# Kernel tuning notes

Measured on AMD Instinct MI355X. Metric: run time of the kernel, lower is better.

Reference implementation:

```python
import jax, jax.numpy as jnp
import numpy as np
from jax import lax

NUM_TAGS = 9
HIDDEN = 768
BATCH = 64
SEQ = 512


def setup_inputs() -> dict:
    key = jax.random.key(0)
    ks = jax.random.split(key, 6)
    hidden = jax.random.normal(ks[0], (BATCH, SEQ, HIDDEN), dtype=jnp.float32)
    labels = jax.random.randint(ks[1], (BATCH, SEQ), 0, NUM_TAGS)  # all >= 0 -> full mask
    weight = jax.random.normal(ks[2], (NUM_TAGS, HIDDEN), dtype=jnp.float32) * 0.02
    bias = jnp.zeros((NUM_TAGS,), dtype=jnp.float32)
    start_transitions = jax.random.normal(ks[3], (NUM_TAGS,), dtype=jnp.float32) * 0.1
    end_transitions = jax.random.normal(ks[4], (NUM_TAGS,), dtype=jnp.float32) * 0.1
    transitions = jax.random.normal(ks[5], (NUM_TAGS, NUM_TAGS), dtype=jnp.float32) * 0.1
    return dict(hidden=hidden, labels=labels, weight=weight, bias=bias,
                start_transitions=start_transitions, end_transitions=end_transitions,
                transitions=transitions)


def _crf_log_likelihood(emissions, tags, mask, start_t, end_t, trans):
    """pytorch-crf log-likelihood, reduction='sum'.
    emissions [B,L,T] float, tags [B,L] int, mask [B,L] bool."""
    # --- numerator: score of the gold path ---
    tag0 = tags[:, 0]
    score0 = start_t[tag0] + jnp.take_along_axis(emissions[:, 0], tag0[:, None], axis=1)[:, 0]

    def num_step(carry, inp):
        score, prev = carry
        em, tg, m = inp  # em [B,T], tg [B], m [B]
        s = trans[prev, tg] + jnp.take_along_axis(em, tg[:, None], axis=1)[:, 0]
        score = score + jnp.where(m, s, jnp.zeros_like(s))
        prev = jnp.where(m, tg, prev)
        return (score, prev), None

    (num_score, last_tag), _ = lax.scan(
        num_step, (score0, tag0),
        (emissions[:, 1:].swapaxes(0, 1), tags[:, 1:].T, mask[:, 1:].T))
    numerator = num_score + end_t[last_tag]

    # --- denominator: forward algorithm (log-sum-exp recurrence) ---
    alpha0 = start_t[None, :] + emissions[:, 0]  # [B,T]

    def den_step(alpha, inp):
        em, m = inp  # em [B,T], m [B]
        nxt = jax.nn.logsumexp(alpha[:, :, None] + trans[None], axis=1) + em
        alpha = jnp.where(m[:, None], nxt, alpha)
        return alpha, None

    alpha, _ = lax.scan(den_step, alpha0,
                        (emissions[:, 1:].swapaxes(0, 1), mask[:, 1:].T))
    denominator = jax.nn.logsumexp(alpha + end_t[None, :], axis=1)

    return jnp.sum(numerator - denominator)


def _viterbi_decode(emissions, mask, start_t, end_t, trans):
    """Max-plus DP + backtrack. Returns padded [B,L] int32 best tag sequence."""
    B, L, T = emissions.shape
    score0 = start_t[None, :] + emissions[:, 0]  # [B,T]
    identity = jnp.arange(T, dtype=jnp.int32)[None, :]  # identity backpointer for masked steps

    def fwd_step(score, inp):
        em, m = inp  # em [B,T], m [B]
        br = score[:, :, None] + trans[None]  # [B,T_prev,T_cur]
        idx = jnp.argmax(br, axis=1).astype(jnp.int32)  # [B,T]
        nxt = jnp.max(br, axis=1) + em
        score = jnp.where(m[:, None], nxt, score)
        idx = jnp.where(m[:, None], idx, identity)
        return score, idx

    final, hist = lax.scan(fwd_step, score0,
                           (emissions[:, 1:].swapaxes(0, 1), mask[:, 1:].T))
    last_tag = jnp.argmax(final + end_t[None, :], axis=1).astype(jnp.int32)  # [B]

    def back_step(tag, idx):  # idx [B,T] backpointers for this position
        prev = jnp.take_along_axis(idx, tag[:, None], axis=1)[:, 0]
        return prev, tag

    first_tag, tags_rev = lax.scan(back_step, last_tag, hist, reverse=True)
    tags = jnp.concatenate([first_tag[None, :], tags_rev], axis=0).T  # [B,L]
    return tags * mask.astype(jnp.int32)


def reference(hidden, labels, weight, bias, start_transitions, end_transitions, transitions):
    mask_full = labels >= 0
    h = hidden[:, 1:-1, :]                       # drop [CLS]/[SEP] positions
    tags = labels[:, 1:-1] * mask_full[:, 1:-1]  # zero out padded labels
    mask = mask_full[:, 1:-1]
    # dropout is identity in eval mode
    emissions = jnp.einsum('blh,th->blt', h, weight) + bias  # [B,L,T]
    llh = _crf_log_likelihood(emissions, tags, mask,
                              start_transitions, end_transitions, transitions)
    tag_seqs = _viterbi_decode(emissions, mask,
                               start_transitions, end_transitions, transitions)
    return -llh, tag_seqs.astype(jnp.float32)
```

## Files before the change

kernel.cpp:

```cpp
#include <hip/hip_runtime.h>
#include <stdint.h>

#define NB 64
#define SEQL 512
#define L 510
#define T 9
#define H 768
#define LN2 0.6931471805599453f

__device__ __forceinline__ float rl(float v, int l) {
  return __uint_as_float(__builtin_amdgcn_readlane(__float_as_uint(v), l));
}

__global__ __launch_bounds__(256, 2) void emis_chunk_kernel(
    const float* __restrict__ hidden, const float* __restrict__ weight,
    const float* __restrict__ bias, const float* __restrict__ trans,
    const float* __restrict__ start_t, const float* __restrict__ end_t,
    const int* __restrict__ labels, float* __restrict__ sel,
    float* __restrict__ em0, float* __restrict__ PdLn, float* __restrict__ Mv,
    unsigned long long* __restrict__ Bp, float* __restrict__ out) {
  __shared__ float4 wl[T * 192];
  __shared__ __align__(16) float s_em[65][12];
  __shared__ __align__(16) float s_ee[65][12];
  __shared__ float s_tr[81];
  const float4* w4 = (const float4*)weight;
  for (int k = threadIdx.x; k < T * 192; k += 256) wl[k] = w4[k];
  if (threadIdx.x < 81) s_tr[threadIdx.x] = trans[threadIdx.x];
  if (blockIdx.x == 0 && threadIdx.x == 0) out[0] = 0.f;
  __syncthreads();
  const int b = blockIdx.x >> 3;
  const int p = blockIdx.x & 7;
  const int row0 = p * 64;
  const int lane = threadIdx.x & 63;
  const int wv = threadIdx.x >> 6;
  const int npair = (wv == 0) ? 9 : 8;
  int i0c, i1c;
  bool v0c, v1c;
  float4 ca[3], cb[3];
  {
    i0c = wv * 16;
    i1c = i0c + 1;
    const int r0 = row0 + i0c, r1 = row0 + i1c;
    v0c = (r0 < L);
    v1c = (r1 < L);
    const int c0 = v0c ? r0 : 0;
    const int c1 = (r1 < L) ? r1 : 0;
    const float4* h0 = (const float4*)(hidden + ((size_t)(b * SEQL + c0 + 1)) * H);
    const float4* h1 = (const float4*)(hidden + ((size_t)(b * SEQL + c1 + 1)) * H);
#pragma unroll
    for (int k = 0; k < 3; ++k) { ca[k] = h0[lane + 64 * k]; cb[k] = h1[lane + 64 * k]; }
  }
#pragma unroll 1
  for (int pr = 0; pr < npair; ++pr) {
    float4 na[3], nb[3];
    int i0n = 0, i1n = 0;
    bool v0n = false, v1n = false;
    if (pr + 1 < npair) {
      const int prn = pr + 1;
      i0n = (prn < 8) ? (wv * 16 + prn * 2) : 64;
      i1n = (prn < 8) ? (i0n + 1) : 64;
      const int r0 = row0 + i0n, r1 = row0 + i1n;
      v0n = (r0 < L);
      v1n = (r1 < L) && (prn < 8);
      const int c0 = v0n ? r0 : 0;
      const int c1 = (r1 < L) ? r1 : 0;
      const float4* h0 = (const float4*)(hidden + ((size_t)(b * SEQL + c0 + 1)) * H);
      const float4* h1 = (const float4*)(hidden + ((size_t)(b * SEQL + c1 + 1)) * H);
#pragma unroll
      for (int k = 0; k < 3; ++k) { na[k] = h0[lane + 64 * k]; nb[k] = h1[lane + 64 * k]; }
    }
    float a0[T], a1[T];
#pragma unroll
    for (int t = 0; t < T; ++t) { a0[t] = 0.f; a1[t] = 0.f; }
#pragma unroll
    for (int t = 0; t < T; ++t) {
#pragma unroll
      for (int k = 0; k < 3; ++k) {
        float4 w = wl[t * 192 + lane + 64 * k];
        a0[t] = fmaf(ca[k].x, w.x, fmaf(ca[k].y, w.y, fmaf(ca[k].z, w.z, fmaf(ca[k].w, w.w, a0[t]))));
        a1[t] = fmaf(cb[k].x, w.x, fmaf(cb[k].y, w.y, fmaf(cb[k].z, w.z, fmaf(cb[k].w, w.w, a1[t]))));
      }
    }
#pragma unroll
    for (int off = 32; off; off >>= 1) {
#pragma unroll
      for (int t = 0; t < T; ++t) {
        a0[t] += __shfl_xor(a0[t], off);
        a1[t] += __shfl_xor(a1[t], off);
      }
    }
    if (lane < 2) {
      const bool vv = lane ? v1c : v0c;
      const int ii = lane ? i1c : i0c;
      if (vv) {
#pragma unroll
        for (int t = 0; t < T; ++t) {
          float v = (lane ? a1[t] : a0[t]) + bias[t];
          s_em[ii][t] = v;
          s_ee[ii][t] = __expf(v);
        }
      }
    }
    if (pr + 1 < npair) {
#pragma unroll
      for (int k = 0; k < 3; ++k) { ca[k] = na[k]; cb[k] = nb[k]; }
      i0c = i0n; i1c = i1n; v0c = v0n; v1c = v1n;
    }
  }
  __syncthreads();
  if (threadIdx.x < 64) {
    const int r = threadIdx.x;
    const int l = row0 + r;
    if (l < L) {
      const int tg = labels[b * SEQL + 1 + l];
      const float e = s_em[r][tg];
      float term;
      if (l == 0) term = start_t[tg] + e;
      else term = s_tr[labels[b * SEQL + l] * 9 + tg] + e;
      sel[b * 512 + l] = term;
      if (l == L - 1) sel[b * 512 + 510] = end_t[tg];
    }
  }
  if (p == 0 && threadIdx.x < 12) em0[b * 12 + threadIdx.x] = s_em[0][threadIdx.x];
  const int cb2 = wv & 1;
  const int sc_ = 2 * p + cb2;
  const int task = b * 16 + sc_;
  const int nt = (sc_ == 15) ? 29 : 32;
  const int base = 1 + 32 * cb2;
  const int i9 = (lane < 9) ? lane : 8;
  if (wv < 2) {
    float E[81];
#pragma unroll
    for (int k = 0; k < 81; ++k) E[k] = __expf(s_tr[k]);
    float R[9];
#pragma unroll
    for (int j = 0; j < 9; ++j) R[j] = __expf(s_tr[i9 * 9 + j]) * s_ee[base][j];
    int iexp = 0;
    for (int t = 1; t < nt; ++t) {
      float Rn[9];
#pragma unroll
      for (int j = 0; j < 9; ++j) {
        float a = R[0] * E[j];
#pragma unroll
        for (int k = 1; k < 9; ++k) a = fmaf(R[k], E[k * 9 + j], a);
        Rn[j] = a;
      }
#pragma unroll
      for (int j = 0; j < 9; ++j) R[j] = Rn[j] * s_ee[base + t][j];
      if ((t & 3) == 0) {
        float mx = R[0];
#pragma unroll
        for (int j = 1; j < 9; ++j) mx = fmaxf(mx, R[j]);
        int ex = (int)((__float_as_uint(mx) >> 23) & 0xff) - 127;
        iexp += ex;
        float sc = __uint_as_float((uint32_t)(127 - ex) << 23);
#pragma unroll
        for (int j = 0; j < 9; ++j) R[j] *= sc;
      }
    }
    if (lane < 9) {
      float ls = (float)iexp * LN2;
#pragma unroll
      for (int j = 0; j < 9; ++j)
        PdLn[(size_t)task * 81 + j * 9 + i9] = __logf(R[j]) + ls;
    }
  } else {
    float t_[81];
#pragma unroll
    for (int k = 0; k < 81; ++k) t_[k] = s_tr[k];
    float V[9];
#pragma unroll
    for (int j = 0; j < 9; ++j) V[j] = s_tr[i9 * 9 + j] + s_em[base][j];
    for (int t = 1; t < nt; ++t) {
      uint32_t lo = 0, hi = 0;
      float Vn[9];
#pragma unroll
      for (int j = 0; j < 9; ++j) {
        float best = V[0] + t_[0 * 9 + j];
        int bi = 0;
#pragma unroll
        for (int k = 1; k < 9; ++k) {
          float v = V[k] + t_[k * 9 + j];
          if (v > best) { best = v; bi = k; }
        }
        Vn[j] = best + s_em[base + t][j];
        if (j < 8) lo |= ((uint32_t)bi) << (4 * j);
        else hi = (uint32_t)bi;
      }
      if (lane < 9)
        Bp[(size_t)task * 288 + t * 9 + i9] =
            (unsigned long long)lo | ((unsigned long long)hi << 32);
#pragma unroll
      for (int j = 0; j < 9; ++j) V[j] = Vn[j];
    }
    if (lane < 9) {
#pragma unroll
      for (int j = 0; j < 9; ++j)
        Mv[(size_t)task * 81 + j * 9 + i9] = V[j];
    }
  }
}

__global__ __launch_bounds__(256) void compose_kernel(
    const float* __restrict__ sel, const float* __restrict__ em0,
    const float* __restrict__ PdLn, const float* __restrict__ Mv,
    const unsigned long long* __restrict__ Bp,
    const float* __restrict__ start_t, const float* __restrict__ end_t,
    float* __restrict__ out) {
  __shared__ __align__(16) float s_pd[16 * 81];
  __shared__ __align__(16) float s_mv[16 * 81];
  __shared__ __align__(16) unsigned long long s_bp[16 * 290];
  __shared__ float s_A[17 * 9];
  __shared__ int s_ch[16][2];
  const int b = blockIdx.x;
  const int tid = threadIdx.x;
  {
    const float4* pdg = (const float4*)(PdLn + (size_t)b * 1296);
    const float4* mvg = (const float4*)(Mv + (size_t)b * 1296);
    for (int k = tid; k < 324; k += 256) {
      ((float4*)s_pd)[k] = pdg[k];
      ((float4*)s_mv)[k] = mvg[k];
    }
    const float4* bpg = (const float4*)(Bp + (size_t)b * 4608);
    for (int k = tid; k < 2304; k += 256) {
      const int s = k / 144, r = k - s * 144;
      ((float4*)&s_bp[s * 290])[r] = bpg[k];
    }
  }
  __syncthreads();
  const int wv = tid >> 6;
  const int lane = tid & 63;
  const int jj = lane < 9 ? lane : 8;

  if (wv == 0) {
    float part_ = 0.f;
    for (int l = lane; l < L; l += 64) part_ += sel[b * 512 + l];
    if (lane == 61) part_ += sel[b * 512 + 510];
#pragma unroll
    for (int off = 32; off; off >>= 1) part_ += __shfl_xor(part_, off);
    float D = start_t[jj] + em0[b * 12 + jj];
    for (int u = 0; u < 16; ++u) {
      const float* col = &s_pd[u * 81 + jj * 9];
      float v0 = rl(D, 0) + col[0], v1 = rl(D, 1) + col[1], v2 = rl(D, 2) + col[2];
      float v3 = rl(D, 3) + col[3], v4 = rl(D, 4) + col[4], v5 = rl(D, 5) + col[5];
      float v6 = rl(D, 6) + col[6], v7 = rl(D, 7) + col[7], v8 = rl(D, 8) + col[8];
      float mx = fmaxf(fmaxf(fmaxf(fmaxf(v0, v1), fmaxf(v2, v3)),
                             fmaxf(fmaxf(v4, v5), fmaxf(v6, v7))), v8);
      float sum = __expf(v0 - mx) + __expf(v1 - mx) + __expf(v2 - mx) +
                  __expf(v3 - mx) + __expf(v4 - mx) + __expf(v5 - mx) +
                  __expf(v6 - mx) + __expf(v7 - mx) + __expf(v8 - mx);
      D = mx + __logf(sum);
    }
    float fe = D + end_t[jj];
    float w0 = rl(fe, 0), w1 = rl(fe, 1), w2 = rl(fe, 2), w3 = rl(fe, 3);
    float w4 = rl(fe, 4), w5 = rl(fe, 5), w6 = rl(fe, 6), w7 = rl(fe, 7), w8 = rl(fe, 8);
    float mx = fmaxf(fmaxf(fmaxf(fmaxf(w0, w1), fmaxf(w2, w3)),
                           fmaxf(fmaxf(w4, w5), fmaxf(w6, w7))), w8);
    float den = mx + __logf(__expf(w0 - mx) + __expf(w1 - mx) + __expf(w2 - mx) +
                            __expf(w3 - mx) + __expf(w4 - mx) + __expf(w5 - mx) +
                            __expf(w6 - mx) + __expf(w7 - mx) + __expf(w8 - mx));
    if (lane == 0) atomicAdd(out, den - part_);
  } else if (wv == 1) {
    float A = start_t[jj] + em0[b * 12 + jj];
    if (lane < 9) s_A[lane] = A;
    for (int u = 0; u < 16; ++u) {
      const float* col = &s_mv[u * 81 + jj * 9];
      float u0 = rl(A, 0) + col[0], u1 = rl(A, 1) + col[1], u2 = rl(A, 2) + col[2];
      float u3 = rl(A, 3) + col[3], u4 = rl(A, 4) + col[4], u5 = rl(A, 5) + col[5];
      float u6 = rl(A, 6) + col[6], u7 = rl(A, 7) + col[7], u8 = rl(A, 8) + col[8];
      A = fmaxf(fmaxf(fmaxf(fmaxf(u0, u1), fmaxf(u2, u3)),
                      fmaxf(fmaxf(u4, u5), fmaxf(u6, u7))), u8);
      if (lane < 9) s_A[(u + 1) * 9 + lane] = A;
    }
    float fv = A + end_t[jj];
    int j = 0;
    {
      float bv = rl(fv, 0);
#pragma unroll
      for (int i = 1; i < 9; ++i) { float v = rl(fv, i); if (v > bv) { bv = v; j = i; } }
    }
    for (int u = 15; u >= 0; --u) {
      float val = s_A[u * 9 + jj] + s_mv[u * 81 + j * 9 + jj];
      int ii = 0;
      float bb = rl(val, 0);
#pragma unroll
      for (int i = 1; i < 9; ++i) { float v = rl(val, i); if (v > bb) { bb = v; ii = i; } }
      if (lane == 0) { s_ch[u][0] = ii; s_ch[u][1] = j; }
      j = ii;
    }
    if (lane == 0) out[1 + (size_t)b * L] = (float)j;
  }
  __syncthreads();
  if (wv == 2 && lane < 16) {
    const int s = lane;
    const int nt = (s == 15) ? 29 : 32;
    const int lb = 32 * s + 1;
    const int i0 = s_ch[s][0];
    int cur = s_ch[s][1];
    float* orow = out + 1 + (size_t)b * L + lb;
    for (int q = nt - 1; q >= 1; --q) {
      orow[q] = (float)cur;
      unsigned long long w = s_bp[s * 290 + q * 9 + i0];
      cur = (int)((w >> (4 * cur)) & 15ULL);
    }
    orow[0] = (float)cur;
  }
}

extern "C" void kernel_launch(void* const* d_in, const int* in_sizes, int n_in,
                              void* d_out, int out_size, void* d_ws, size_t ws_size,
                              hipStream_t stream) {
  const float* hidden  = (const float*)d_in[0];
  const int*   labels  = (const int*)d_in[1];
  const float* weight  = (const float*)d_in[2];
  const float* bias    = (const float*)d_in[3];
  const float* start_t = (const float*)d_in[4];
  const float* end_t   = (const float*)d_in[5];
  const float* trans   = (const float*)d_in[6];
  float* out = (float*)d_out;

  unsigned long long* Bp = (unsigned long long*)d_ws;
  float* sel  = (float*)(Bp + (size_t)1024 * 288);
  float* em0  = sel + (size_t)64 * 512;
  float* PdLn = em0 + 768;
  float* Mv   = PdLn + (size_t)1024 * 81;

  emis_chunk_kernel<<<512, 256, 0, stream>>>(hidden, weight, bias, trans,
                                             start_t, end_t, labels,
                                             sel, em0, PdLn, Mv, Bp, out);
  compose_kernel<<<NB, 256, 0, stream>>>(sel, em0, PdLn, Mv, Bp,
                                         start_t, end_t, out);
}
```

Before: 222.6 us.

## Fuse compose kernel into chunk kernel via last-block-done atomic counters

Merges the second (compose) kernel into the first by having each of the 8 blocks per batch increment a per-batch counter after a threadfence. The last block to finish runs the compose work in reused shared memory. A second counter finalizes the global loss sum. This removes one kernel launch and the inter-kernel gap. In exchange it adds a memset launch, atomics and fences, and a serial tail on the last-arriving block.

```diff
diff --git a/kernel.cpp b/kernel.cpp
--- a/kernel.cpp
+++ b/kernel.cpp
@@ -18,15 +18,17 @@
     const float* __restrict__ start_t, const float* __restrict__ end_t,
     const int* __restrict__ labels, float* __restrict__ sel,
     float* __restrict__ em0, float* __restrict__ PdLn, float* __restrict__ Mv,
-    unsigned long long* __restrict__ Bp, float* __restrict__ out) {
-  __shared__ float4 wl[T * 192];
-  __shared__ __align__(16) float s_em[65][12];
-  __shared__ __align__(16) float s_ee[65][12];
-  __shared__ float s_tr[81];
+    unsigned long long* __restrict__ Bp, int* __restrict__ cnt,
+    int* __restrict__ cnt2, float* __restrict__ acc, float* __restrict__ out) {
+  __shared__ __align__(16) unsigned char smem[48240];
+  __shared__ int s_flag;
+  float4* wl = (float4*)smem;
+  float (*s_em)[12] = (float(*)[12])(smem + 27648);
+  float (*s_ee)[12] = (float(*)[12])(smem + 30768);
+  float* s_tr = (float*)(smem + 33888);
   const float4* w4 = (const float4*)weight;
   for (int k = threadIdx.x; k < T * 192; k += 256) wl[k] = w4[k];
   if (threadIdx.x < 81) s_tr[threadIdx.x] = trans[threadIdx.x];
-  if (blockIdx.x == 0 && threadIdx.x == 0) out[0] = 0.f;
   __syncthreads();
   const int b = blockIdx.x >> 3;
   const int p = blockIdx.x & 7;
@@ -199,20 +201,21 @@
         Mv[(size_t)task * 81 + j * 9 + i9] = V[j];
     }
   }
-}
-
-__global__ __launch_bounds__(256) void compose_kernel(
-    const float* __restrict__ sel, const float* __restrict__ em0,
-    const float* __restrict__ PdLn, const float* __restrict__ Mv,
-    const unsigned long long* __restrict__ Bp,
-    const float* __restrict__ start_t, const float* __restrict__ end_t,
-    float* __restrict__ out) {
-  __shared__ __align__(16) float s_pd[16 * 81];
-  __shared__ __align__(16) float s_mv[16 * 81];
-  __shared__ __align__(16) unsigned long long s_bp[16 * 290];
-  __shared__ float s_A[17 * 9];
-  __shared__ int s_ch[16][2];
-  const int b = blockIdx.x;
+  __threadfence();
+  __syncthreads();
+  if (threadIdx.x == 0) {
+    int old = atomicAdd(&cnt[b], 1);
+    s_flag = (old == 7) ? 1 : 0;
+  }
+  __syncthreads();
+  if (!s_flag) return;
+  __threadfence();
+
+  float* s_pd = (float*)smem;
+  float* s_mv = (float*)(smem + 5184);
+  unsigned long long* s_bp = (unsigned long long*)(smem + 10368);
+  float* s_A = (float*)(smem + 47488);
+  int* s_ch = (int*)(smem + 48100);
   const int tid = threadIdx.x;
   {
     const float4* pdg = (const float4*)(PdLn + (size_t)b * 1296);
@@ -228,9 +231,6 @@
     }
   }
   __syncthreads();
-  const int wv = tid >> 6;
-  const int lane = tid & 63;
-  const int jj = lane < 9 ? lane : 8;
 
   if (wv == 0) {
     float part_ = 0.f;
@@ -238,9 +238,9 @@
     if (lane == 61) part_ += sel[b * 512 + 510];
 #pragma unroll
     for (int off = 32; off; off >>= 1) part_ += __shfl_xor(part_, off);
-    float D = start_t[jj] + em0[b * 12 + jj];
+    float D = start_t[i9] + em0[b * 12 + i9];
     for (int u = 0; u < 16; ++u) {
-      const float* col = &s_pd[u * 81 + jj * 9];
+      const float* col = &s_pd[u * 81 + i9 * 9];
       float v0 = rl(D, 0) + col[0], v1 = rl(D, 1) + col[1], v2 = rl(D, 2) + col[2];
       float v3 = rl(D, 3) + col[3], v4 = rl(D, 4) + col[4], v5 = rl(D, 5) + col[5];
       float v6 = rl(D, 6) + col[6], v7 = rl(D, 7) + col[7], v8 = rl(D, 8) + col[8];
@@ -251,7 +251,7 @@
                   __expf(v6 - mx) + __expf(v7 - mx) + __expf(v8 - mx);
       D = mx + __logf(sum);
     }
-    float fe = D + end_t[jj];
+    float fe = D + end_t[i9];
     float w0 = rl(fe, 0), w1 = rl(fe, 1), w2 = rl(fe, 2), w3 = rl(fe, 3);
     float w4 = rl(fe, 4), w5 = rl(fe, 5), w6 = rl(fe, 6), w7 = rl(fe, 7), w8 = rl(fe, 8);
     float mx = fmaxf(fmaxf(fmaxf(fmaxf(w0, w1), fmaxf(w2, w3)),
@@ -259,12 +259,20 @@
     float den = mx + __logf(__expf(w0 - mx) + __expf(w1 - mx) + __expf(w2 - mx) +
                             __expf(w3 - mx) + __expf(w4 - mx) + __expf(w5 - mx) +
                             __expf(w6 - mx) + __expf(w7 - mx) + __expf(w8 - mx));
-    if (lane == 0) atomicAdd(out, den - part_);
+    if (lane == 0) {
+      atomicAdd(acc, den - part_);
+      __threadfence();
+      int o2 = atomicAdd(cnt2, 1);
+      if (o2 == 63) {
+        float total = atomicAdd(acc, 0.0f);
+        out[0] = total;
+      }
+    }
   } else if (wv == 1) {
-    float A = start_t[jj] + em0[b * 12 + jj];
+    float A = start_t[i9] + em0[b * 12 + i9];
     if (lane < 9) s_A[lane] = A;
     for (int u = 0; u < 16; ++u) {
-      const float* col = &s_mv[u * 81 + jj * 9];
+      const float* col = &s_mv[u * 81 + i9 * 9];
       float u0 = rl(A, 0) + col[0], u1 = rl(A, 1) + col[1], u2 = rl(A, 2) + col[2];
       float u3 = rl(A, 3) + col[3], u4 = rl(A, 4) + col[4], u5 = rl(A, 5) + col[5];
       float u6 = rl(A, 6) + col[6], u7 = rl(A, 7) + col[7], u8 = rl(A, 8) + col[8];
@@ -272,7 +280,7 @@
                       fmaxf(fmaxf(u4, u5), fmaxf(u6, u7))), u8);
       if (lane < 9) s_A[(u + 1) * 9 + lane] = A;
     }
-    float fv = A + end_t[jj];
+    float fv = A + end_t[i9];
     int j = 0;
     {
       float bv = rl(fv, 0);
@@ -280,12 +288,12 @@
       for (int i = 1; i < 9; ++i) { float v = rl(fv, i); if (v > bv) { bv = v; j = i; } }
     }
     for (int u = 15; u >= 0; --u) {
-      float val = s_A[u * 9 + jj] + s_mv[u * 81 + j * 9 + jj];
+      float val = s_A[u * 9 + i9] + s_mv[u * 81 + j * 9 + i9];
       int ii = 0;
       float bb = rl(val, 0);
 #pragma unroll
       for (int i = 1; i < 9; ++i) { float v = rl(val, i); if (v > bb) { bb = v; ii = i; } }
-      if (lane == 0) { s_ch[u][0] = ii; s_ch[u][1] = j; }
+      if (lane == 0) { s_ch[u * 2] = ii; s_ch[u * 2 + 1] = j; }
       j = ii;
     }
     if (lane == 0) out[1 + (size_t)b * L] = (float)j;
@@ -293,12 +301,12 @@
   __syncthreads();
   if (wv == 2 && lane < 16) {
     const int s = lane;
-    const int nt = (s == 15) ? 29 : 32;
+    const int ntc = (s == 15) ? 29 : 32;
     const int lb = 32 * s + 1;
-    const int i0 = s_ch[s][0];
-    int cur = s_ch[s][1];
+    const int i0 = s_ch[s * 2];
+    int cur = s_ch[s * 2 + 1];
     float* orow = out + 1 + (size_t)b * L + lb;
-    for (int q = nt - 1; q >= 1; --q) {
+    for (int q = ntc - 1; q >= 1; --q) {
       orow[q] = (float)cur;
       unsigned long long w = s_bp[s * 290 + q * 9 + i0];
       cur = (int)((w >> (4 * cur)) & 15ULL);
@@ -319,15 +327,18 @@
   const float* trans   = (const float*)d_in[6];
   float* out = (float*)d_out;
 
-  unsigned long long* Bp = (unsigned long long*)d_ws;
+  int*   cnt  = (int*)d_ws;
+  int*   cnt2 = cnt + 64;
+  float* acc  = (float*)(cnt + 65);
+  unsigned long long* Bp = (unsigned long long*)((char*)d_ws + 512);
   float* sel  = (float*)(Bp + (size_t)1024 * 288);
   float* em0  = sel + (size_t)64 * 512;
   float* PdLn = em0 + 768;
   float* Mv   = PdLn + (size_t)1024 * 81;
 
+  hipMemsetAsync(d_ws, 0, 512, stream);
   emis_chunk_kernel<<<512, 256, 0, stream>>>(hidden, weight, bias, trans,
                                              start_t, end_t, labels,
-                                             sel, em0, PdLn, Mv, Bp, out);
-  compose_kernel<<<NB, 256, 0, stream>>>(sel, em0, PdLn, Mv, Bp,
-                                         start_t, end_t, out);
+                                             sel, em0, PdLn, Mv, Bp,
+                                             cnt, cnt2, acc, out);
 }
```

Result: slower. 258.8 us (+16.3%).

## Split emission-chunk kernel into one block per 32-row chunk

Applied to the files above, without the earlier changes.

Doubles the grid from 512 to 1024 blocks, so each block computes emissions for 32 rows instead of 64 and handles a single chunk task. Within that task, wave 0 runs the forward product and wave 1 runs Viterbi; waves 2-3 sit idle during the scan phase. Launch bounds rise to 4 blocks per SM to allow higher occupancy. The aim is shorter serial per-block work and better latency hiding, at the cost of reloading the weight matrix into LDS twice as often and leaving half the waves idle in the recurrence.

```diff
diff --git a/kernel.cpp b/kernel.cpp
--- a/kernel.cpp
+++ b/kernel.cpp
@@ -12,7 +12,7 @@
   return __uint_as_float(__builtin_amdgcn_readlane(__float_as_uint(v), l));
 }
 
-__global__ __launch_bounds__(256, 2) void emis_chunk_kernel(
+__global__ __launch_bounds__(256, 4) void emis_chunk_kernel(
     const float* __restrict__ hidden, const float* __restrict__ weight,
     const float* __restrict__ bias, const float* __restrict__ trans,
     const float* __restrict__ start_t, const float* __restrict__ end_t,
@@ -20,27 +20,27 @@
     float* __restrict__ em0, float* __restrict__ PdLn, float* __restrict__ Mv,
     unsigned long long* __restrict__ Bp, float* __restrict__ out) {
   __shared__ float4 wl[T * 192];
-  __shared__ __align__(16) float s_em[65][12];
-  __shared__ __align__(16) float s_ee[65][12];
+  __shared__ __align__(16) float s_em[33][12];
+  __shared__ __align__(16) float s_ee[33][12];
   __shared__ float s_tr[81];
   const float4* w4 = (const float4*)weight;
   for (int k = threadIdx.x; k < T * 192; k += 256) wl[k] = w4[k];
   if (threadIdx.x < 81) s_tr[threadIdx.x] = trans[threadIdx.x];
   if (blockIdx.x == 0 && threadIdx.x == 0) out[0] = 0.f;
   __syncthreads();
-  const int b = blockIdx.x >> 3;
-  const int p = blockIdx.x & 7;
-  const int row0 = p * 64;
+  const int b = blockIdx.x >> 4;
+  const int c = blockIdx.x & 15;
+  const int R0 = c * 32;
   const int lane = threadIdx.x & 63;
   const int wv = threadIdx.x >> 6;
-  const int npair = (wv == 0) ? 9 : 8;
+  const int npair = (wv == 0) ? 5 : 4;
   int i0c, i1c;
   bool v0c, v1c;
   float4 ca[3], cb[3];
   {
-    i0c = wv * 16;
+    i0c = wv * 8;
     i1c = i0c + 1;
-    const int r0 = row0 + i0c, r1 = row0 + i1c;
+    const int r0 = R0 + i0c, r1 = R0 + i1c;
     v0c = (r0 < L);
     v1c = (r1 < L);
     const int c0 = v0c ? r0 : 0;
@@ -57,11 +57,11 @@
     bool v0n = false, v1n = false;
     if (pr + 1 < npair) {
       const int prn = pr + 1;
-      i0n = (prn < 8) ? (wv * 16 + prn * 2) : 64;
-      i1n = (prn < 8) ? (i0n + 1) : 64;
-      const int r0 = row0 + i0n, r1 = row0 + i1n;
+      i0n = (prn < 4) ? (wv * 8 + prn * 2) : 32;
+      i1n = (prn < 4) ? (i0n + 1) : 32;
+      const int r0 = R0 + i0n, r1 = R0 + i1n;
       v0n = (r0 < L);
-      v1n = (r1 < L) && (prn < 8);
+      v1n = (r1 < L) && (prn < 4);
       const int c0 = v0n ? r0 : 0;
       const int c1 = (r1 < L) ? r1 : 0;
       const float4* h0 = (const float4*)(hidden + ((size_t)(b * SEQL + c0 + 1)) * H);
@@ -108,9 +108,9 @@
     }
   }
   __syncthreads();
-  if (threadIdx.x < 64) {
+  if (threadIdx.x < 32) {
     const int r = threadIdx.x;
-    const int l = row0 + r;
+    const int l = R0 + r;
     if (l < L) {
       const int tg = labels[b * SEQL + 1 + l];
       const float e = s_em[r][tg];
@@ -121,20 +121,17 @@
       if (l == L - 1) sel[b * 512 + 510] = end_t[tg];
     }
   }
-  if (p == 0 && threadIdx.x < 12) em0[b * 12 + threadIdx.x] = s_em[0][threadIdx.x];
-  const int cb2 = wv & 1;
-  const int sc_ = 2 * p + cb2;
-  const int task = b * 16 + sc_;
-  const int nt = (sc_ == 15) ? 29 : 32;
-  const int base = 1 + 32 * cb2;
+  if (c == 0 && threadIdx.x < 12) em0[b * 12 + threadIdx.x] = s_em[0][threadIdx.x];
+  const int task = b * 16 + c;
+  const int nt = (c == 15) ? 29 : 32;
   const int i9 = (lane < 9) ? lane : 8;
-  if (wv < 2) {
+  if (wv == 0) {
     float E[81];
 #pragma unroll
     for (int k = 0; k < 81; ++k) E[k] = __expf(s_tr[k]);
     float R[9];
 #pragma unroll
-    for (int j = 0; j < 9; ++j) R[j] = __expf(s_tr[i9 * 9 + j]) * s_ee[base][j];
+    for (int j = 0; j < 9; ++j) R[j] = __expf(s_tr[i9 * 9 + j]) * s_ee[1][j];
     int iexp = 0;
     for (int t = 1; t < nt; ++t) {
       float Rn[9];
@@ -146,7 +143,7 @@
         Rn[j] = a;
       }
 #pragma unroll
-      for (int j = 0; j < 9; ++j) R[j] = Rn[j] * s_ee[base + t][j];
+      for (int j = 0; j < 9; ++j) R[j] = Rn[j] * s_ee[1 + t][j];
       if ((t & 3) == 0) {
         float mx = R[0];
 #pragma unroll
@@ -164,13 +161,13 @@
       for (int j = 0; j < 9; ++j)
         PdLn[(size_t)task * 81 + j * 9 + i9] = __logf(R[j]) + ls;
     }
-  } else {
+  } else if (wv == 1) {
     float t_[81];
 #pragma unroll
     for (int k = 0; k < 81; ++k) t_[k] = s_tr[k];
     float V[9];
 #pragma unroll
-    for (int j = 0; j < 9; ++j) V[j] = s_tr[i9 * 9 + j] + s_em[base][j];
+    for (int j = 0; j < 9; ++j) V[j] = s_tr[i9 * 9 + j] + s_em[1][j];
     for (int t = 1; t < nt; ++t) {
       uint32_t lo = 0, hi = 0;
       float Vn[9];
@@ -183,7 +180,7 @@
           float v = V[k] + t_[k * 9 + j];
           if (v > best) { best = v; bi = k; }
         }
-        Vn[j] = best + s_em[base + t][j];
+        Vn[j] = best + s_em[1 + t][j];
         if (j < 8) lo |= ((uint32_t)bi) << (4 * j);
         else hi = (uint32_t)bi;
       }
@@ -325,9 +322,9 @@
   float* PdLn = em0 + 768;
   float* Mv   = PdLn + (size_t)1024 * 81;
 
-  emis_chunk_kernel<<<512, 256, 0, stream>>>(hidden, weight, bias, trans,
-                                             start_t, end_t, labels,
-                                             sel, em0, PdLn, Mv, Bp, out);
+  emis_chunk_kernel<<<1024, 256, 0, stream>>>(hidden, weight, bias, trans,
+                                              start_t, end_t, labels,
+                                              sel, em0, PdLn, Mv, Bp, out);
   compose_kernel<<<NB, 256, 0, stream>>>(sel, em0, PdLn, Mv, Bp,
                                          start_t, end_t, out);
 }
```

After: 304.0 us. 36.6% more time.
